# Optimization experiments

Measured on AMD Instinct MI355X. Metric: run time of the kernel, lower is better.

The kernel has to match this reference:

```python
import jax, jax.numpy as jnp
import numpy as np
from jax import lax

B, H, N, D = 8, 8, 4096, 64
NUM_LANDMARKS = 256
PINV_ITERS = 6
KERNEL = 33


def moore_penrose_iter_pinv(x, iters=PINV_ITERS):
    # x: [b, h, m, m]
    abs_x = jnp.abs(x)
    col = abs_x.sum(axis=-1)
    row = abs_x.sum(axis=-2)
    z = jnp.swapaxes(x, -1, -2) / (jnp.max(col) * jnp.max(row))
    I = jnp.eye(x.shape[-1], dtype=x.dtype)
    for _ in range(iters):
        xz = x @ z
        z = 0.25 * z @ (13.0 * I - xz @ (15.0 * I - xz @ (7.0 * I - xz)))
    return z


def setup_inputs() -> dict:
    key = jax.random.key(0)
    ks = jax.random.split(key, 10)
    inp = {
        'q': jax.random.normal(ks[0], (B, H, N, D), dtype=jnp.float32),
        'k': jax.random.normal(ks[1], (B, H, N, D), dtype=jnp.float32),
        'v': jax.random.normal(ks[2], (B, H, N, D), dtype=jnp.float32),
        'Wsim1': jax.random.uniform(ks[3], (H, H), dtype=jnp.float32),
        'Wsim2': jax.random.uniform(ks[4], (H, H), dtype=jnp.float32),
        'Wsim3': jax.random.uniform(ks[5], (H, H), dtype=jnp.float32),
        'Wattn1': jax.random.uniform(ks[6], (H, H), dtype=jnp.float32),
        'Wattn2': jax.random.uniform(ks[7], (H, H), dtype=jnp.float32),
        'Wattn3': jax.random.uniform(ks[8], (H, H), dtype=jnp.float32),
        'conv_w': jax.random.normal(ks[9], (H, H, KERNEL, 1), dtype=jnp.float32) * 0.05,
    }
    return inp


def reference(q, k, v, Wsim1, Wsim2, Wsim3, Wattn1, Wattn2, Wattn3, conv_w):
    b, h, n, d = q.shape
    # m = max(12, min(num_landmarks, int((sqrt(kn) + sqrt(qn)) // 2))) -> 64 for n=4096
    m = max(12, min(NUM_LANDMARKS, int((n ** 0.5 + n ** 0.5) // 2)))
    l = -(-n // m)  # ceil(n / m); n % m == 0 here so no padding branch

    # landmarks: group-sum over l consecutive tokens, divided by l
    q_l = q.reshape(b, h, m, l, d).sum(axis=3) / l  # [b,h,m,d]
    k_l = k.reshape(b, h, m, l, d).sum(axis=3) / l  # [b,h,m,d]

    sim1 = jnp.einsum('bhid,bhjd->bhij', q, k_l)    # [b,h,n,m]
    sim2 = jnp.einsum('bhid,bhjd->bhij', q_l, k_l)  # [b,h,m,m]
    sim3 = jnp.einsum('bhid,bhjd->bhij', q_l, k)    # [b,h,m,n]

    # talking-head mixing on sims
    sim1 = jnp.einsum('bhij,hk->bkij', sim1, Wsim1)
    sim2 = jnp.einsum('bhij,hk->bkij', sim2, Wsim2)
    sim3 = jnp.einsum('bhij,hk->bkij', sim3, Wsim3)

    attn1 = jax.nn.softmax(sim1, axis=-1)
    attn2 = jax.nn.softmax(sim2, axis=-1)
    attn3 = jax.nn.softmax(sim3, axis=-1)

    attn2_inv = moore_penrose_iter_pinv(attn2, PINV_ITERS)

    # talking-head mixing on attns
    attn1 = jnp.einsum('bhij,hk->bkij', attn1, Wattn1)
    attn2_inv = jnp.einsum('bhij,hk->bkij', attn2_inv, Wattn2)
    attn3 = jnp.einsum('bhij,hk->bkij', attn3, Wattn3)

    out = attn1 @ (attn2_inv @ (attn3 @ v))  # [b,h,n,d]

    # residual depthwise-ish conv over (n, d) treating heads as channels
    pad = KERNEL // 2
    res = lax.conv_general_dilated(
        v, conv_w,
        window_strides=(1, 1),
        padding=[(pad, pad), (0, 0)],
        dimension_numbers=('NCHW', 'OIHW', 'NCHW'))
    out = out + res
    return out
```

## Files before the change

### kernel.cpp

```cpp
#include <hip/hip_runtime.h>
#include <cstddef>
#include <cstdint>

constexpr int cB = 8, cH = 8, cN = 4096, cD = 64, cM = 64, cL = 64;

__global__ void k_landmarks(const float* __restrict__ q, const float* __restrict__ k,
                            float* __restrict__ ql, float* __restrict__ kl) {
  int bm = blockIdx.x;
  int bh = bm >> 6, m = bm & 63;
  int d = threadIdx.x;
  size_t base = ((size_t)bh * cN + (size_t)m * cL) * cD + d;
  float sq = 0.f, sk = 0.f;
  for (int t = 0; t < cL; ++t) {
    sq += q[base + (size_t)t * cD];
    sk += k[base + (size_t)t * cD];
  }
  size_t ob = ((size_t)bh * cM + m) * cD + d;
  ql[ob] = sq * (1.0f / cL);
  kl[ob] = sk * (1.0f / cL);
}

__global__ void __launch_bounds__(256) k_sim2(const float* __restrict__ ql,
                                              const float* __restrict__ kl,
                                              const float* __restrict__ Wsim2,
                                              float* __restrict__ attn2,
                                              unsigned int* __restrict__ scal) {
  __shared__ float qs[64][65];
  __shared__ float ks[64][65];
  __shared__ float acc[64 * 65];
  int b = blockIdx.x >> 3, kk = blockIdx.x & 7;
  int tid = threadIdx.x;
  for (int idx = tid; idx < 64 * 64; idx += 256)
    acc[(idx >> 6) * 65 + (idx & 63)] = 0.f;
  int ri = (tid >> 4) * 4, ci = (tid & 15) * 4;
  for (int h = 0; h < 8; ++h) {
    __syncthreads();
    const float* qg = ql + (size_t)(b * 8 + h) * 4096;
    const float* kg = kl + (size_t)(b * 8 + h) * 4096;
    for (int idx = tid; idx < 4096; idx += 256) {
      qs[idx >> 6][idx & 63] = qg[idx];
      ks[idx >> 6][idx & 63] = kg[idx];
    }
    __syncthreads();
    float w = Wsim2[h * 8 + kk];
    float s[4][4] = {};
    for (int d = 0; d < 64; ++d) {
      float a0 = qs[ri][d], a1 = qs[ri + 1][d], a2 = qs[ri + 2][d], a3 = qs[ri + 3][d];
      float b0 = ks[ci][d], b1 = ks[ci + 1][d], b2 = ks[ci + 2][d], b3 = ks[ci + 3][d];
      s[0][0] += a0 * b0; s[0][1] += a0 * b1; s[0][2] += a0 * b2; s[0][3] += a0 * b3;
      s[1][0] += a1 * b0; s[1][1] += a1 * b1; s[1][2] += a1 * b2; s[1][3] += a1 * b3;
      s[2][0] += a2 * b0; s[2][1] += a2 * b1; s[2][2] += a2 * b2; s[2][3] += a2 * b3;
      s[3][0] += a3 * b0; s[3][1] += a3 * b1; s[3][2] += a3 * b2; s[3][3] += a3 * b3;
    }
    #pragma unroll
    for (int x = 0; x < 4; ++x)
      #pragma unroll
      for (int y = 0; y < 4; ++y)
        acc[(ri + x) * 65 + ci + y] += w * s[x][y];
  }
  __syncthreads();
  if (tid < 64) {
    float mx = -1e30f;
    for (int j = 0; j < 64; ++j) mx = fmaxf(mx, acc[tid * 65 + j]);
    float s = 0.f;
    for (int j = 0; j < 64; ++j) {
      float e = expf(acc[tid * 65 + j] - mx);
      acc[tid * 65 + j] = e;
      s += e;
    }
    float inv = 1.0f / s;
    float rs = 0.f;
    for (int j = 0; j < 64; ++j) {
      float p = acc[tid * 65 + j] * inv;
      acc[tid * 65 + j] = p;
      rs += p;
    }
    atomicMax(scal + 1, __float_as_uint(rs));
  }
  __syncthreads();
  if (tid < 64) {
    float cs = 0.f;
    for (int i = 0; i < 64; ++i) cs += acc[i * 65 + tid];
    atomicMax(scal + 0, __float_as_uint(cs));
  }
  __syncthreads();
  float* op = attn2 + (size_t)(b * 8 + kk) * 4096;
  for (int idx = tid; idx < 4096; idx += 256)
    op[idx] = acc[(idx >> 6) * 65 + (idx & 63)];
}

__global__ void k_klT(float* __restrict__ kl) {
  __shared__ float t[64 * 65];
  int bh = blockIdx.x, tid = threadIdx.x;
  float* p = kl + (size_t)bh * 4096;
  for (int idx = tid; idx < 4096; idx += 256)
    t[(idx >> 6) * 65 + (idx & 63)] = p[idx];
  __syncthreads();
  for (int idx = tid; idx < 4096; idx += 256)
    p[idx] = t[(idx & 63) * 65 + (idx >> 6)];
}

__device__ __forceinline__ void mm64(float* __restrict__ Dst, const float* S,
                                     float c0, float c1, const float* __restrict__ P,
                                     const float* __restrict__ Q, int tid) {
  int ri = (tid >> 4) * 4, ci = (tid & 15) * 4;
  float s[4][4] = {};
  for (int k = 0; k < 64; ++k) {
    float a0 = P[(ri + 0) * 65 + k], a1 = P[(ri + 1) * 65 + k];
    float a2 = P[(ri + 2) * 65 + k], a3 = P[(ri + 3) * 65 + k];
    float b0 = Q[k * 65 + ci + 0], b1 = Q[k * 65 + ci + 1];
    float b2 = Q[k * 65 + ci + 2], b3 = Q[k * 65 + ci + 3];
    s[0][0] += a0 * b0; s[0][1] += a0 * b1; s[0][2] += a0 * b2; s[0][3] += a0 * b3;
    s[1][0] += a1 * b0; s[1][1] += a1 * b1; s[1][2] += a1 * b2; s[1][3] += a1 * b3;
    s[2][0] += a2 * b0; s[2][1] += a2 * b1; s[2][2] += a2 * b2; s[2][3] += a2 * b3;
    s[3][0] += a3 * b0; s[3][1] += a3 * b1; s[3][2] += a3 * b2; s[3][3] += a3 * b3;
  }
  #pragma unroll
  for (int x = 0; x < 4; ++x)
    #pragma unroll
    for (int y = 0; y < 4; ++y) {
      float r = c1 * s[x][y];
      if (S) r += c0 * S[(ri + x) * 65 + ci + y];
      Dst[(ri + x) * 65 + ci + y] = r;
    }
}

__global__ void __launch_bounds__(256) k_pinv(const float* __restrict__ attn2,
                                              float* __restrict__ attn2inv,
                                              const unsigned int* __restrict__ scal) {
  __shared__ float bufs[5][64 * 65];
  float* X = bufs[0];
  float* Z = bufs[1];
  float* T1 = bufs[2];
  float* T2 = bufs[3];
  float* T3 = bufs[4];
  int tid = threadIdx.x;
  const float* xg = attn2 + (size_t)blockIdx.x * 4096;
  for (int idx = tid; idx < 4096; idx += 256)
    X[(idx >> 6) * 65 + (idx & 63)] = xg[idx];
  float denom = __uint_as_float(scal[0]) * __uint_as_float(scal[1]);
  float invd = 1.0f / denom;
  __syncthreads();
  for (int idx = tid; idx < 4096; idx += 256) {
    int i = idx >> 6, j = idx & 63;
    Z[i * 65 + j] = X[j * 65 + i] * invd;
  }
  __syncthreads();
  for (int it = 0; it < 6; ++it) {
    mm64(T1, nullptr, 0.f, 1.f, X, Z, tid);          __syncthreads();
    mm64(T2, T1, 7.f, -1.f, T1, T1, tid);            __syncthreads();
    mm64(T3, T1, 15.f, -1.f, T1, T2, tid);           __syncthreads();
    mm64(T2, Z, 13.f * 0.25f, -0.25f, Z, T3, tid);   __syncthreads();
    float* tmp = Z; Z = T2; T2 = tmp;
  }
  float* og = attn2inv + (size_t)blockIdx.x * 4096;
  for (int idx = tid; idx < 4096; idx += 256)
    og[idx] = Z[(idx >> 6) * 65 + (idx & 63)];
}

__global__ void k_mix_heads64(const float* __restrict__ in, const float* __restrict__ W,
                              float* __restrict__ out) {
  int b = blockIdx.x >> 3, k2 = blockIdx.x & 7;
  int tid = threadIdx.x;
  __shared__ float w[8];
  if (tid < 8) w[tid] = W[tid * 8 + k2];
  __syncthreads();
  const float* ib = in + (size_t)b * 8 * 4096;
  float* ob = out + ((size_t)b * 8 + k2) * 4096;
  for (int idx = tid; idx < 4096; idx += 256) {
    float s = 0.f;
    #pragma unroll
    for (int k = 0; k < 8; ++k) s += ib[(size_t)k * 4096 + idx] * w[k];
    ob[idx] = s;
  }
}

__global__ void __launch_bounds__(512) k_sim3(const float* __restrict__ ql,
                                              const float* __restrict__ kg,
                                              const float* __restrict__ Wsim3,
                                              float* __restrict__ sim3m) {
  __shared__ float qls[64 * 65];
  __shared__ float ksT[64 * 36];
  __shared__ float w3[64];
  int b = blockIdx.x >> 7, jt = blockIdx.x & 127;
  int j0 = jt * 32, tid = threadIdx.x;
  if (tid < 64) w3[tid] = Wsim3[tid];
  int i = tid >> 3, jb = (tid & 7) * 4;
  float acc[8][4] = {};
  for (int h = 0; h < 8; ++h) {
    __syncthreads();
    const float* qg = ql + (size_t)(b * 8 + h) * 4096;
    for (int idx = tid; idx < 4096; idx += 512)
      qls[(idx >> 6) * 65 + (idx & 63)] = qg[idx];
    const float* kp = kg + ((size_t)(b * 8 + h) * cN + j0) * 64;
    for (int idx = tid; idx < 2048; idx += 512) {
      int j = idx >> 6, d = idx & 63;
      ksT[d * 36 + j] = kp[idx];
    }
    __syncthreads();
    float s[4] = {};
    for (int d = 0; d < 64; ++d) {
      float a = qls[i * 65 + d];
      float4 kv = *(const float4*)&ksT[d * 36 + jb];
      s[0] += a * kv.x; s[1] += a * kv.y; s[2] += a * kv.z; s[3] += a * kv.w;
    }
    #pragma unroll
    for (int k = 0; k < 8; ++k) {
      float w = w3[h * 8 + k];
      #pragma unroll
      for (int c = 0; c < 4; ++c) acc[k][c] += w * s[c];
    }
  }
  #pragma unroll
  for (int k = 0; k < 8; ++k) {
    float* op = sim3m + ((size_t)((b * 8 + k) * 64 + i)) * cN + j0 + jb;
    *(float4*)op = make_float4(acc[k][0], acc[k][1], acc[k][2], acc[k][3]);
  }
}

__global__ void k_stats3(const float* __restrict__ sim3m, float* __restrict__ rmax,
                         float* __restrict__ rsum) {
  int row = blockIdx.x;
  const float* rp = sim3m + (size_t)row * cN;
  int tid = threadIdx.x;
  float vv[16];
  float mx = -1e30f;
  #pragma unroll
  for (int t = 0; t < 16; ++t) {
    vv[t] = rp[tid + t * 256];
    mx = fmaxf(mx, vv[t]);
  }
  __shared__ float red[8];
  for (int off = 32; off > 0; off >>= 1) mx = fmaxf(mx, __shfl_down(mx, off));
  if ((tid & 63) == 0) red[tid >> 6] = mx;
  __syncthreads();
  mx = fmaxf(fmaxf(red[0], red[1]), fmaxf(red[2], red[3]));
  float s = 0.f;
  #pragma unroll
  for (int t = 0; t < 16; ++t) s += expf(vv[t] - mx);
  for (int off = 32; off > 0; off >>= 1) s += __shfl_down(s, off);
  __syncthreads();
  if ((tid & 63) == 0) red[4 + (tid >> 6)] = s;
  __syncthreads();
  if (tid == 0) {
    rmax[row] = mx;
    rsum[row] = red[4] + red[5] + red[6] + red[7];
  }
}

__global__ void __launch_bounds__(256) k_smx3(float* __restrict__ sim3m,
                                              const float* __restrict__ rmax,
                                              const float* __restrict__ rsum,
                                              const float* __restrict__ Wattn3) {
  __shared__ float w[64];
  int tid = threadIdx.x;
  if (tid < 64) w[tid] = Wattn3[tid];
  __syncthreads();
  int gid = blockIdx.x * 256 + tid;
  int j = gid & 4095;
  int i = (gid >> 12) & 63;
  int b = gid >> 18;
  float p[8];
  #pragma unroll
  for (int k = 0; k < 8; ++k) {
    int row = (b * 8 + k) * 64 + i;
    p[k] = expf(sim3m[(size_t)row * cN + j] - rmax[row]) / rsum[row];
  }
  #pragma unroll
  for (int k2 = 0; k2 < 8; ++k2) {
    float t = 0.f;
    #pragma unroll
    for (int k = 0; k < 8; ++k) t += p[k] * w[k * 8 + k2];
    int row = (b * 8 + k2) * 64 + i;
    sim3m[(size_t)row * cN + j] = t;
  }
}

__global__ void __launch_bounds__(256) k_t3(const float* __restrict__ attn3f,
                                            const float* __restrict__ v,
                                            float* __restrict__ T3p) {
  __shared__ float As[64][65];
  __shared__ float Vs[64][68];
  int bh = blockIdx.x >> 2, chunk = blockIdx.x & 3;
  int tid = threadIdx.x;
  int ri = (tid >> 4) * 4, ci = (tid & 15) * 4;
  float acc[4][4] = {};
  for (int jt = chunk * 16; jt < chunk * 16 + 16; ++jt) {
    __syncthreads();
    const float* ap = attn3f + (size_t)bh * 64 * cN + jt * 64;
    for (int idx = tid; idx < 4096; idx += 256)
      As[idx >> 6][idx & 63] = ap[(size_t)(idx >> 6) * cN + (idx & 63)];
    const float* vp = v + ((size_t)bh * cN + jt * 64) * 64;
    for (int idx = tid; idx < 4096; idx += 256)
      Vs[idx >> 6][idx & 63] = vp[idx];
    __syncthreads();
    for (int j = 0; j < 64; ++j) {
      float a0 = As[ri][j], a1 = As[ri + 1][j], a2 = As[ri + 2][j], a3 = As[ri + 3][j];
      float b0 = Vs[j][ci], b1 = Vs[j][ci + 1], b2 = Vs[j][ci + 2], b3 = Vs[j][ci + 3];
      acc[0][0] += a0 * b0; acc[0][1] += a0 * b1; acc[0][2] += a0 * b2; acc[0][3] += a0 * b3;
      acc[1][0] += a1 * b0; acc[1][1] += a1 * b1; acc[1][2] += a1 * b2; acc[1][3] += a1 * b3;
      acc[2][0] += a2 * b0; acc[2][1] += a2 * b1; acc[2][2] += a2 * b2; acc[2][3] += a2 * b3;
      acc[3][0] += a3 * b0; acc[3][1] += a3 * b1; acc[3][2] += a3 * b2; acc[3][3] += a3 * b3;
    }
  }
  float* op = T3p + ((size_t)chunk * 64 + bh) * 4096;
  #pragma unroll
  for (int x = 0; x < 4; ++x)
    #pragma unroll
    for (int y = 0; y < 4; ++y)
      op[(ri + x) * 64 + ci + y] = acc[x][y];
}

__global__ void __launch_bounds__(256) k_t2(const float* __restrict__ attn2m,
                                            const float* __restrict__ T3p,
                                            float* __restrict__ T2) {
  __shared__ float As[64][65];
  __shared__ float Bs[64][68];
  int bh = blockIdx.x, tid = threadIdx.x;
  const float* ap = attn2m + (size_t)bh * 4096;
  for (int idx = tid; idx < 4096; idx += 256) {
    As[idx >> 6][idx & 63] = ap[idx];
    float s = 0.f;
    #pragma unroll
    for (int c = 0; c < 4; ++c) s += T3p[((size_t)c * 64 + bh) * 4096 + idx];
    Bs[idx >> 6][idx & 63] = s;
  }
  __syncthreads();
  int ri = (tid >> 4) * 4, ci = (tid & 15) * 4;
  float acc[4][4] = {};
  for (int j = 0; j < 64; ++j) {
    float a0 = As[ri][j], a1 = As[ri + 1][j], a2 = As[ri + 2][j], a3 = As[ri + 3][j];
    float b0 = Bs[j][ci], b1 = Bs[j][ci + 1], b2 = Bs[j][ci + 2], b3 = Bs[j][ci + 3];
    acc[0][0] += a0 * b0; acc[0][1] += a0 * b1; acc[0][2] += a0 * b2; acc[0][3] += a0 * b3;
    acc[1][0] += a1 * b0; acc[1][1] += a1 * b1; acc[1][2] += a1 * b2; acc[1][3] += a1 * b3;
    acc[2][0] += a2 * b0; acc[2][1] += a2 * b1; acc[2][2] += a2 * b2; acc[2][3] += a2 * b3;
    acc[3][0] += a3 * b0; acc[3][1] += a3 * b1; acc[3][2] += a3 * b2; acc[3][3] += a3 * b3;
  }
  #pragma unroll
  for (int x = 0; x < 4; ++x)
    #pragma unroll
    for (int y = 0; y < 4; ++y)
      T2[(size_t)bh * 4096 + (ri + x) * 64 + ci + y] = acc[x][y];
}

__global__ void __launch_bounds__(256) k_conv(const float* __restrict__ v,
                                              const float* __restrict__ cw,
                                              float* __restrict__ out) {
  __shared__ float wl[2112];
  int tid = threadIdx.x;
  for (int idx = tid; idx < 2112; idx += 256) {
    int o = idx / 264, r = idx % 264, i = r / 33, t = r % 33;
    wl[i * 264 + t * 8 + o] = cw[idx];
  }
  __syncthreads();
  int d = tid & 63;
  int sub = tid >> 6;
  int b = blockIdx.x >> 8;
  int n0 = (blockIdx.x & 255) * 16 + sub * 4;
  float acc[8][4] = {};
  for (int i = 0; i < 8; ++i) {
    const float* vp = v + ((size_t)(b * 8 + i) * cN) * 64 + d;
    float win[36];
    #pragma unroll
    for (int t = 0; t < 36; ++t) {
      int nn = n0 - 16 + t;
      win[t] = (nn >= 0 && nn < cN) ? vp[(size_t)nn * 64] : 0.f;
    }
    #pragma unroll
    for (int t = 0; t < 33; ++t) {
      float4 w0 = *(const float4*)&wl[i * 264 + t * 8];
      float4 w1 = *(const float4*)&wl[i * 264 + t * 8 + 4];
      #pragma unroll
      for (int u = 0; u < 4; ++u) {
        float val = win[t + u];
        acc[0][u] += val * w0.x; acc[1][u] += val * w0.y;
        acc[2][u] += val * w0.z; acc[3][u] += val * w0.w;
        acc[4][u] += val * w1.x; acc[5][u] += val * w1.y;
        acc[6][u] += val * w1.z; acc[7][u] += val * w1.w;
      }
    }
  }
  #pragma unroll
  for (int o = 0; o < 8; ++o) {
    float* op = out + ((size_t)(b * 8 + o) * cN + n0) * 64 + d;
    #pragma unroll
    for (int u = 0; u < 4; ++u) op[(size_t)u * 64] = acc[o][u];
  }
}

__device__ __forceinline__ void dot64_4x4(const float* __restrict__ A,
                                          const float* __restrict__ Bm, int jb,
                                          float s[4][4]) {
  #pragma unroll
  for (int dc = 0; dc < 16; ++dc) {
    float4 kv0 = *(const float4*)&Bm[(dc * 4 + 0) * 68 + jb];
    float4 kv1 = *(const float4*)&Bm[(dc * 4 + 1) * 68 + jb];
    float4 kv2 = *(const float4*)&Bm[(dc * 4 + 2) * 68 + jb];
    float4 kv3 = *(const float4*)&Bm[(dc * 4 + 3) * 68 + jb];
    #pragma unroll
    for (int r = 0; r < 4; ++r) {
      float4 af = *(const float4*)&A[r * 68 + dc * 4];
      s[r][0] += af.x * kv0.x; s[r][1] += af.x * kv0.y; s[r][2] += af.x * kv0.z; s[r][3] += af.x * kv0.w;
      s[r][0] += af.y * kv1.x; s[r][1] += af.y * kv1.y; s[r][2] += af.y * kv1.z; s[r][3] += af.y * kv1.w;
      s[r][0] += af.z * kv2.x; s[r][1] += af.z * kv2.y; s[r][2] += af.z * kv2.z; s[r][3] += af.z * kv2.w;
      s[r][0] += af.w * kv3.x; s[r][1] += af.w * kv3.y; s[r][2] += af.w * kv3.z; s[r][3] += af.w * kv3.w;
    }
  }
}

__device__ __forceinline__ void stage_q(float* __restrict__ dst,
                                        const float4* __restrict__ src, int tid) {
  int sr = tid >> 4, sc = (tid & 15) * 4;
  float4 a = src[tid];
  float4 b = src[tid + 512];
  float4 c = src[tid + 1024];
  float4 d = src[tid + 1536];
  *(float4*)&dst[sr * 68 + sc] = a;
  *(float4*)&dst[(32 + sr) * 68 + sc] = b;
  *(float4*)&dst[(64 + sr) * 68 + sc] = c;
  *(float4*)&dst[(96 + sr) * 68 + sc] = d;
}

__device__ __forceinline__ void stage_l(float* __restrict__ dst,
                                        const float4* __restrict__ src, int tid) {
  int sr = tid >> 4, sc = (tid & 15) * 4;
  float4 a = src[tid];
  float4 b = src[tid + 512];
  *(float4*)&dst[sr * 68 + sc] = a;
  *(float4*)&dst[(32 + sr) * 68 + sc] = b;
}

__global__ void __launch_bounds__(512) k_final(const float* __restrict__ q,
                                               const float* __restrict__ klT,
                                               const float* __restrict__ T2,
                                               const float* __restrict__ Wsim1,
                                               const float* __restrict__ Wattn1,
                                               float* __restrict__ out) {
  __shared__ float SB[2 * 128 * 68 + 2 * 64 * 68];
  __shared__ float ws1[64], wa1[64];
  constexpr int PITCH = 68, QBUF = 128 * 68, LBUF = 64 * 68;
  float* Q0 = SB;
  float* L0 = SB + 2 * QBUF;
  int b = blockIdx.x >> 5, i0 = (blockIdx.x & 31) * 128;
  int tid = threadIdx.x;
  if (tid < 64) { ws1[tid] = Wsim1[tid]; wa1[tid] = Wattn1[tid]; }
  int jb = (tid & 15) * 4, r0 = (tid >> 4) * 4;

  float sim[8][4][4] = {};

  const float4* qb = (const float4*)(q + ((size_t)(b * 8) * cN + i0) * 64);
  const float4* kb = (const float4*)(klT + (size_t)(b * 8) * 4096);
  const float4* tb = (const float4*)(T2 + (size_t)(b * 8) * 4096);

  stage_q(Q0, qb, tid);
  stage_l(L0, kb, tid);
  __syncthreads();

  for (int h = 0; h < 7; ++h) {
    int p = h & 1, pn = p ^ 1;
    stage_q(Q0 + pn * QBUF, qb + (size_t)(h + 1) * 65536, tid);
    stage_l(L0 + pn * LBUF, kb + (size_t)(h + 1) * 1024, tid);
    float s[4][4] = {};
    dot64_4x4(Q0 + p * QBUF + r0 * PITCH, L0 + p * LBUF, jb, s);
    #pragma unroll
    for (int kq = 0; kq < 8; ++kq) {
      float wv = ws1[h * 8 + kq];
      #pragma unroll
      for (int r = 0; r < 4; ++r)
        #pragma unroll
        for (int c = 0; c < 4; ++c) sim[kq][r][c] += wv * s[r][c];
    }
    __syncthreads();
  }

  {
    stage_l(L0, tb, tid);
    float s[4][4] = {};
    dot64_4x4(Q0 + 1 * QBUF + r0 * PITCH, L0 + 1 * LBUF, jb, s);
    #pragma unroll
    for (int kq = 0; kq < 8; ++kq) {
      float wv = ws1[56 + kq];
      #pragma unroll
      for (int r = 0; r < 4; ++r)
        #pragma unroll
        for (int c = 0; c < 4; ++c) sim[kq][r][c] += wv * s[r][c];
    }
    #pragma unroll
    for (int kq = 0; kq < 8; ++kq) {
      #pragma unroll
      for (int r = 0; r < 4; ++r) {
        float mx = fmaxf(fmaxf(sim[kq][r][0], sim[kq][r][1]),
                         fmaxf(sim[kq][r][2], sim[kq][r][3]));
        mx = fmaxf(mx, __shfl_xor(mx, 1)); mx = fmaxf(mx, __shfl_xor(mx, 2));
        mx = fmaxf(mx, __shfl_xor(mx, 4)); mx = fmaxf(mx, __shfl_xor(mx, 8));
        float sm = 0.f;
        #pragma unroll
        for (int c = 0; c < 4; ++c) {
          sim[kq][r][c] = expf(sim[kq][r][c] - mx);
          sm += sim[kq][r][c];
        }
        sm += __shfl_xor(sm, 1); sm += __shfl_xor(sm, 2);
        sm += __shfl_xor(sm, 4); sm += __shfl_xor(sm, 8);
        float inv = 1.0f / sm;
        #pragma unroll
        for (int c = 0; c < 4; ++c) sim[kq][r][c] *= inv;
      }
    }
    #pragma unroll
    for (int r = 0; r < 4; ++r)
      #pragma unroll
      for (int c = 0; c < 4; ++c) {
        float t[8];
        #pragma unroll
        for (int k2 = 0; k2 < 8; ++k2) {
          float a = 0.f;
          #pragma unroll
          for (int kk = 0; kk < 8; ++kk) a += sim[kk][r][c] * wa1[kk * 8 + k2];
          t[k2] = a;
        }
        #pragma unroll
        for (int k2 = 0; k2 < 8; ++k2) sim[k2][r][c] = t[k2];
      }
    #pragma unroll
    for (int r = 0; r < 4; ++r)
      *(float4*)&Q0[(r0 + r) * PITCH + jb] =
          make_float4(sim[0][r][0], sim[0][r][1], sim[0][r][2], sim[0][r][3]);
    __syncthreads();
  }

  #pragma unroll
  for (int k2 = 0; k2 < 8; ++k2) {
    int p = k2 & 1, pn = p ^ 1;
    if (k2 < 7) {
      stage_l(L0 + pn * LBUF, tb + (size_t)(k2 + 1) * 1024, tid);
      #pragma unroll
      for (int r = 0; r < 4; ++r)
        *(float4*)&Q0[pn * QBUF + (r0 + r) * PITCH + jb] =
            make_float4(sim[k2 + 1][r][0], sim[k2 + 1][r][1],
                        sim[k2 + 1][r][2], sim[k2 + 1][r][3]);
    }
    float o[4][4] = {};
    dot64_4x4(Q0 + p * QBUF + r0 * PITCH, L0 + p * LBUF, jb, o);
    #pragma unroll
    for (int r = 0; r < 4; ++r) {
      float* op = out + ((size_t)(b * 8 + k2) * cN + i0 + r0 + r) * 64 + jb;
      float4 e = *(float4*)op;
      e.x += o[r][0]; e.y += o[r][1]; e.z += o[r][2]; e.w += o[r][3];
      *(float4*)op = e;
    }
    if (k2 < 7) __syncthreads();
  }
}

extern "C" void kernel_launch(void* const* d_in, const int* in_sizes, int n_in,
                              void* d_out, int out_size, void* d_ws, size_t ws_size,
                              hipStream_t stream) {
  const float* q = (const float*)d_in[0];
  const float* k = (const float*)d_in[1];
  const float* v = (const float*)d_in[2];
  const float* Wsim1 = (const float*)d_in[3];
  const float* Wsim2 = (const float*)d_in[4];
  const float* Wsim3 = (const float*)d_in[5];
  const float* Wattn1 = (const float*)d_in[6];
  const float* Wattn2 = (const float*)d_in[7];
  const float* Wattn3 = (const float*)d_in[8];
  const float* cw = (const float*)d_in[9];
  float* out = (float*)d_out;
  float* ws = (float*)d_ws;

  float* ql       = ws + 0;
  float* kl       = ws + 262144;
  float* attn2    = ws + 524288;
  float* attn2inv = ws + 786432;
  float* attn2m   = ws + 1048576;
  float* T2       = ws + 1310720;
  float* rmax     = ws + 1572864;
  float* rsum     = ws + 1576960;
  unsigned int* scal = (unsigned int*)(ws + 1581056);
  float* T3p      = ws + 1581120;
  float* sim3m = out;

  hipMemsetAsync(scal, 0, 8, stream);
  k_landmarks<<<dim3(4096), dim3(64), 0, stream>>>(q, k, ql, kl);
  k_sim2<<<dim3(64), dim3(256), 0, stream>>>(ql, kl, Wsim2, attn2, scal);
  k_klT<<<dim3(64), dim3(256), 0, stream>>>(kl);
  k_pinv<<<dim3(64), dim3(256), 0, stream>>>(attn2, attn2inv, scal);
  k_mix_heads64<<<dim3(64), dim3(256), 0, stream>>>(attn2inv, Wattn2, attn2m);
  k_sim3<<<dim3(1024), dim3(512), 0, stream>>>(ql, k, Wsim3, sim3m);
  k_stats3<<<dim3(4096), dim3(256), 0, stream>>>(sim3m, rmax, rsum);
  k_smx3<<<dim3(8192), dim3(256), 0, stream>>>(sim3m, rmax, rsum, Wattn3);
  k_t3<<<dim3(256), dim3(256), 0, stream>>>(sim3m, v, T3p);
  k_t2<<<dim3(64), dim3(256), 0, stream>>>(attn2m, T3p, T2);
  k_conv<<<dim3(2048), dim3(256), 0, stream>>>(v, cw, out);
  k_final<<<dim3(256), dim3(512), 0, stream>>>(q, kl, T2, Wsim1, Wattn1, out);
}
```

Measured before the change: 838.1 us.

## Fuse sim3 softmax stats and head-mix into one LDS-staged kernel; widen conv tile

Replaces the separate row-stats and softmax/head-mix kernels with one kernel per (b,i) that stages all 8 head rows (128KB) in shared memory, computes max/sum per row, then applies softmax and the Wattn3 mixing from shared memory. This removes one full global read of sim3 and the rmax/rsum round trip. Each block now uses a large shared-memory footprint, which limits occupancy to about one block per CU. The conv kernel also processes 8 outputs per thread instead of 4 and takes a branch-free load path for interior windows, reducing redundant window loads at the cost of more registers.

```diff
diff --git a/kernel.cpp b/kernel.cpp
--- a/kernel.cpp
+++ b/kernel.cpp
@@ -218,61 +218,55 @@
   }
 }
 
-__global__ void k_stats3(const float* __restrict__ sim3m, float* __restrict__ rmax,
-                         float* __restrict__ rsum) {
-  int row = blockIdx.x;
-  const float* rp = sim3m + (size_t)row * cN;
-  int tid = threadIdx.x;
-  float vv[16];
-  float mx = -1e30f;
-  #pragma unroll
-  for (int t = 0; t < 16; ++t) {
-    vv[t] = rp[tid + t * 256];
-    mx = fmaxf(mx, vv[t]);
-  }
+__global__ void __launch_bounds__(512) k_smxt3(float* __restrict__ sim3m,
+                                               const float* __restrict__ Wattn3) {
+  __shared__ float S[8][4096];
+  __shared__ float w[64];
   __shared__ float red[8];
-  for (int off = 32; off > 0; off >>= 1) mx = fmaxf(mx, __shfl_down(mx, off));
-  if ((tid & 63) == 0) red[tid >> 6] = mx;
-  __syncthreads();
-  mx = fmaxf(fmaxf(red[0], red[1]), fmaxf(red[2], red[3]));
-  float s = 0.f;
-  #pragma unroll
-  for (int t = 0; t < 16; ++t) s += expf(vv[t] - mx);
-  for (int off = 32; off > 0; off >>= 1) s += __shfl_down(s, off);
-  __syncthreads();
-  if ((tid & 63) == 0) red[4 + (tid >> 6)] = s;
-  __syncthreads();
-  if (tid == 0) {
-    rmax[row] = mx;
-    rsum[row] = red[4] + red[5] + red[6] + red[7];
-  }
-}
-
-__global__ void __launch_bounds__(256) k_smx3(float* __restrict__ sim3m,
-                                              const float* __restrict__ rmax,
-                                              const float* __restrict__ rsum,
-                                              const float* __restrict__ Wattn3) {
-  __shared__ float w[64];
+  int b = blockIdx.x >> 6, i = blockIdx.x & 63;
   int tid = threadIdx.x;
   if (tid < 64) w[tid] = Wattn3[tid];
-  __syncthreads();
-  int gid = blockIdx.x * 256 + tid;
-  int j = gid & 4095;
-  int i = (gid >> 12) & 63;
-  int b = gid >> 18;
-  float p[8];
-  #pragma unroll
+  float m[8], inv[8];
   for (int k = 0; k < 8; ++k) {
-    int row = (b * 8 + k) * 64 + i;
-    p[k] = expf(sim3m[(size_t)row * cN + j] - rmax[row]) / rsum[row];
-  }
-  #pragma unroll
-  for (int k2 = 0; k2 < 8; ++k2) {
-    float t = 0.f;
-    #pragma unroll
-    for (int k = 0; k < 8; ++k) t += p[k] * w[k * 8 + k2];
-    int row = (b * 8 + k2) * 64 + i;
-    sim3m[(size_t)row * cN + j] = t;
+    float* rp = sim3m + ((size_t)((b * 8 + k) * 64 + i)) * cN;
+    float vv[8];
+    float mx = -1e30f;
+    #pragma unroll
+    for (int t = 0; t < 8; ++t) {
+      vv[t] = rp[tid + t * 512];
+      S[k][tid + t * 512] = vv[t];
+      mx = fmaxf(mx, vv[t]);
+    }
+    for (int off = 32; off > 0; off >>= 1) mx = fmaxf(mx, __shfl_down(mx, off));
+    __syncthreads();
+    if ((tid & 63) == 0) red[tid >> 6] = mx;
+    __syncthreads();
+    mx = fmaxf(fmaxf(fmaxf(red[0], red[1]), fmaxf(red[2], red[3])),
+               fmaxf(fmaxf(red[4], red[5]), fmaxf(red[6], red[7])));
+    float s = 0.f;
+    #pragma unroll
+    for (int t = 0; t < 8; ++t) s += expf(vv[t] - mx);
+    for (int off = 32; off > 0; off >>= 1) s += __shfl_down(s, off);
+    __syncthreads();
+    if ((tid & 63) == 0) red[tid >> 6] = s;
+    __syncthreads();
+    float st = red[0] + red[1] + red[2] + red[3] +
+               red[4] + red[5] + red[6] + red[7];
+    m[k] = mx;
+    inv[k] = 1.0f / st;
+  }
+  __syncthreads();
+  for (int j = tid; j < 4096; j += 512) {
+    float p[8];
+    #pragma unroll
+    for (int k = 0; k < 8; ++k) p[k] = expf(S[k][j] - m[k]) * inv[k];
+    #pragma unroll
+    for (int k2 = 0; k2 < 8; ++k2) {
+      float t = 0.f;
+      #pragma unroll
+      for (int k = 0; k < 8; ++k) t += p[k] * w[k * 8 + k2];
+      sim3m[((size_t)((b * 8 + k2) * 64 + i)) * cN + j] = t;
+    }
   }
 }
 
@@ -355,23 +349,30 @@
   __syncthreads();
   int d = tid & 63;
   int sub = tid >> 6;
-  int b = blockIdx.x >> 8;
-  int n0 = (blockIdx.x & 255) * 16 + sub * 4;
-  float acc[8][4] = {};
+  int b = blockIdx.x >> 7;
+  int n0 = (blockIdx.x & 127) * 32 + sub * 8;
+  int lo = n0 - 16;
+  bool interior = (lo >= 0) && (lo + 39 < cN);
+  float acc[8][8] = {};
   for (int i = 0; i < 8; ++i) {
     const float* vp = v + ((size_t)(b * 8 + i) * cN) * 64 + d;
-    float win[36];
-    #pragma unroll
-    for (int t = 0; t < 36; ++t) {
-      int nn = n0 - 16 + t;
-      win[t] = (nn >= 0 && nn < cN) ? vp[(size_t)nn * 64] : 0.f;
+    float win[40];
+    if (interior) {
+      #pragma unroll
+      for (int t = 0; t < 40; ++t) win[t] = vp[(size_t)(lo + t) * 64];
+    } else {
+      #pragma unroll
+      for (int t = 0; t < 40; ++t) {
+        int nn = lo + t;
+        win[t] = (nn >= 0 && nn < cN) ? vp[(size_t)nn * 64] : 0.f;
+      }
     }
     #pragma unroll
     for (int t = 0; t < 33; ++t) {
       float4 w0 = *(const float4*)&wl[i * 264 + t * 8];
       float4 w1 = *(const float4*)&wl[i * 264 + t * 8 + 4];
       #pragma unroll
-      for (int u = 0; u < 4; ++u) {
+      for (int u = 0; u < 8; ++u) {
         float val = win[t + u];
         acc[0][u] += val * w0.x; acc[1][u] += val * w0.y;
         acc[2][u] += val * w0.z; acc[3][u] += val * w0.w;
@@ -384,7 +385,7 @@
   for (int o = 0; o < 8; ++o) {
     float* op = out + ((size_t)(b * 8 + o) * cN + n0) * 64 + d;
     #pragma unroll
-    for (int u = 0; u < 4; ++u) op[(size_t)u * 64] = acc[o][u];
+    for (int u = 0; u < 8; ++u) op[(size_t)u * 64] = acc[o][u];
   }
 }
 
@@ -574,8 +575,6 @@
   float* attn2inv = ws + 786432;
   float* attn2m   = ws + 1048576;
   float* T2       = ws + 1310720;
-  float* rmax     = ws + 1572864;
-  float* rsum     = ws + 1576960;
   unsigned int* scal = (unsigned int*)(ws + 1581056);
   float* T3p      = ws + 1581120;
   float* sim3m = out;
@@ -587,10 +586,9 @@
   k_pinv<<<dim3(64), dim3(256), 0, stream>>>(attn2, attn2inv, scal);
   k_mix_heads64<<<dim3(64), dim3(256), 0, stream>>>(attn2inv, Wattn2, attn2m);
   k_sim3<<<dim3(1024), dim3(512), 0, stream>>>(ql, k, Wsim3, sim3m);
-  k_stats3<<<dim3(4096), dim3(256), 0, stream>>>(sim3m, rmax, rsum);
-  k_smx3<<<dim3(8192), dim3(256), 0, stream>>>(sim3m, rmax, rsum, Wattn3);
+  k_smxt3<<<dim3(512), dim3(512), 0, stream>>>(sim3m, Wattn3);
   k_t3<<<dim3(256), dim3(256), 0, stream>>>(sim3m, v, T3p);
   k_t2<<<dim3(64), dim3(256), 0, stream>>>(attn2m, T3p, T2);
-  k_conv<<<dim3(2048), dim3(256), 0, stream>>>(v, cw, out);
+  k_conv<<<dim3(1024), dim3(256), 0, stream>>>(v, cw, out);
   k_final<<<dim3(256), dim3(512), 0, stream>>>(q, kl, T2, Wsim1, Wattn1, out);
 }
```

Measured after the change: 811.8 us. -3.1%, faster.
